# Optimization experiments

Hardware: AMD Instinct MI355X
Metric: run time of the kernel (lower is better)

Reference implementation:

```python
import jax, jax.numpy as jnp
import numpy as np


def setup_inputs() -> dict:
    key = jax.random.key(0)
    B, N, D = 8, 2048, 512
    put = jax.random.normal(key, (B, N, D), dtype=jnp.float32)
    return {"put": put, "k": 16}


def reference(put, k):
    # put: [B, N, D]; k: python int
    B, N, _ = put.shape
    # squared-norm expansion of pairwise Euclidean distance
    xx = jnp.sum(put * put, axis=2, keepdims=True)            # [B, N, 1]
    gram = jnp.einsum('bnd,bmd->bnm', put, put)               # [B, N, N]
    dist2 = xx + jnp.swapaxes(xx, 1, 2) - 2.0 * gram          # [B, N, N]
    dist = jnp.sqrt(jnp.clip(dist2, 0.0))                     # clamp(min=0).sqrt()

    # k nearest (smallest distance): top_k of negated distances
    _, inc = jax.lax.top_k(-dist, k)                          # [B, N, k] int32

    # binary adjacency: out[b, j, inc[b, j, :]] = 1 (vectorized scatter)
    b_idx = jnp.arange(B)[:, None, None]                      # [B,1,1]
    r_idx = jnp.arange(N)[None, :, None]                      # [1,N,1]
    out = jnp.zeros_like(dist).at[b_idx, r_idx, inc].set(1.0)
    return out
```

## Files before the change

kernel.cpp:

```cpp
#include <hip/hip_runtime.h>
#include <cstdint>

#define NN 2048
#define DD 512
#define NB 8
#define NCAND 24

using ull = unsigned long long;
typedef __attribute__((ext_vector_type(8))) short bf16x8;
typedef __attribute__((ext_vector_type(4))) float f32x4;

#define GLOAD_LDS16(g, l)                                                      \
  __builtin_amdgcn_global_load_lds(                                            \
      (const __attribute__((address_space(1))) unsigned int*)(g),              \
      (__attribute__((address_space(3))) unsigned int*)(l), 16, 0, 0)

__device__ inline unsigned short f2bf(float f) {
  unsigned u = __float_as_uint(f);
  unsigned r = u + 0x7FFFu + ((u >> 16) & 1u);
  return (unsigned short)(r >> 16);
}

#define CEX(a, i, j)                                                           \
  {                                                                            \
    unsigned lo_ = min(a[i], a[j]), hi_ = max(a[i], a[j]);                     \
    a[i] = lo_;                                                                \
    a[j] = hi_;                                                                \
  }

__device__ __forceinline__ void sort8(unsigned (&a)[8]) {
  CEX(a, 0, 1) CEX(a, 2, 3) CEX(a, 4, 5) CEX(a, 6, 7)
  CEX(a, 0, 2) CEX(a, 1, 3) CEX(a, 4, 6) CEX(a, 5, 7)
  CEX(a, 1, 2) CEX(a, 5, 6)
  CEX(a, 0, 4) CEX(a, 1, 5) CEX(a, 2, 6) CEX(a, 3, 7)
  CEX(a, 2, 4) CEX(a, 3, 5)
  CEX(a, 1, 2) CEX(a, 3, 4) CEX(a, 5, 6)
}

__device__ __forceinline__ void clean16(unsigned (&r)[16]) {
#pragma unroll
  for (int d = 8; d >= 1; d >>= 1) {
#pragma unroll
    for (int i = 0; i < 16; ++i)
      if ((i & d) == 0) CEX(r, i, i + d)
  }
}

__device__ __forceinline__ void merge16_full(const unsigned (&a)[8],
                                             const unsigned (&b)[8],
                                             unsigned (&r)[16]) {
#pragma unroll
  for (int i = 0; i < 8; ++i) { r[i] = a[i]; r[15 - i] = b[i]; }
  clean16(r);
}

__device__ __forceinline__ void top16(unsigned (&a)[16], const unsigned (&b)[16]) {
  unsigned t[16];
#pragma unroll
  for (int i = 0; i < 16; ++i) t[i] = min(a[i], b[15 - i]);
  clean16(t);
#pragma unroll
  for (int i = 0; i < 16; ++i) a[i] = t[i];
}

__device__ __forceinline__ void load8(unsigned (&a)[8], const unsigned short* p,
                                      unsigned c0) {
  uint4 u = *(const uint4*)p;
  a[0] = (u.x << 16) | c0;
  a[1] = (u.x & 0xFFFF0000u) | (c0 + 1);
  a[2] = (u.y << 16) | (c0 + 2);
  a[3] = (u.y & 0xFFFF0000u) | (c0 + 3);
  a[4] = (u.z << 16) | (c0 + 4);
  a[5] = (u.z & 0xFFFF0000u) | (c0 + 5);
  a[6] = (u.w << 16) | (c0 + 6);
  a[7] = (u.w & 0xFFFF0000u) | (c0 + 7);
}

__device__ __forceinline__ void sel_write(const unsigned short* S,
                                          unsigned* __restrict__ Kws, int b,
                                          int rowbase, int tile, int colbase,
                                          int t) {
  const int row = t >> 1, half = t & 1;
  const unsigned short* Sr = S + row * 136 + half * 64;
  const unsigned cb = (unsigned)(colbase + half * 64);
  unsigned m[16], s0[8], s1[8], n16[16];
  load8(s0, Sr + 0, cb + 0);
  load8(s1, Sr + 8, cb + 8);
  sort8(s0); sort8(s1);
  merge16_full(s0, s1, m);
#pragma unroll
  for (int c = 16; c < 64; c += 16) {
    load8(s0, Sr + c, cb + c);
    load8(s1, Sr + c + 8, cb + c + 8);
    sort8(s0); sort8(s1);
    merge16_full(s0, s1, n16);
    top16(m, n16);
  }
  unsigned o[16];
#pragma unroll
  for (int i = 0; i < 16; ++i) o[i] = (unsigned)__shfl_xor((int)m[i], 1, 64);
  top16(m, o);
  if (half == 0) {
    unsigned* dst = Kws + ((size_t)(b * NN + rowbase + row) * 16 + tile) * 12;
#pragma unroll
    for (int i = 0; i < 12; ++i) dst[i] = m[i];
  }
}

__global__ __launch_bounds__(256) void knn_prep(const float* __restrict__ put,
                                                float* __restrict__ norms32,
                                                unsigned short* __restrict__ bhalf) {
  const int row  = blockIdx.x * 4 + (threadIdx.x >> 6);
  const int lane = threadIdx.x & 63;
  const float* p = put + (size_t)row * DD + lane * 8;
  float4 x0 = ((const float4*)p)[0];
  float4 x1 = ((const float4*)p)[1];
  double s = (double)x0.x * (double)x0.x + (double)x0.y * (double)x0.y +
             (double)x0.z * (double)x0.z + (double)x0.w * (double)x0.w +
             (double)x1.x * (double)x1.x + (double)x1.y * (double)x1.y +
             (double)x1.z * (double)x1.z + (double)x1.w * (double)x1.w;
  uint4 v;
  v.x = (unsigned)f2bf(x0.x) | ((unsigned)f2bf(x0.y) << 16);
  v.y = (unsigned)f2bf(x0.z) | ((unsigned)f2bf(x0.w) << 16);
  v.z = (unsigned)f2bf(x1.x) | ((unsigned)f2bf(x1.y) << 16);
  v.w = (unsigned)f2bf(x1.z) | ((unsigned)f2bf(x1.w) << 16);
  *((uint4*)(bhalf + (size_t)row * DD) + lane) = v;
#pragma unroll
  for (int m = 1; m < 64; m <<= 1) s += __shfl_xor(s, m, 64);
  if (lane == 0) norms32[row] = (float)s;
}

__global__ __launch_bounds__(256, 3) void knn_gemm(
    const unsigned short* __restrict__ bhalf,
    const float* __restrict__ norms32,
    unsigned* __restrict__ Kws) {
  __shared__ unsigned short smem[17408];
  unsigned short* As = smem;
  unsigned short* Bs = smem + 4096;

  int idx = blockIdx.x;
  int jt = 0;
  while (idx >= 16 - jt) { idx -= 16 - jt; ++jt; }
  const int mt = jt + idx;

  const int t    = threadIdx.x;
  const int lane = t & 63;
  const int wv   = t >> 6;
  const int q    = lane >> 4;
  const int l15  = lane & 15;
  const int wrow = wv >> 1, wcol = wv & 1;
  const int m0 = mt * 128;
  const int j0 = jt * 128;
  const int b  = blockIdx.y;

  const unsigned short* pb = bhalf + (size_t)b * NN * DD;

  const int rloc = lane >> 2;
  const int kcg  = (lane & 3) ^ ((lane >> 3) & 3);
  const int i0 = 2 * wv, i1 = 2 * wv + 1;
  const unsigned short* gA0 = pb + (size_t)(j0 + 16 * i0 + rloc) * DD + kcg * 8;
  const unsigned short* gA1 = pb + (size_t)(j0 + 16 * i1 + rloc) * DD + kcg * 8;
  const unsigned short* gB0 = pb + (size_t)(m0 + 16 * i0 + rloc) * DD + kcg * 8;
  const unsigned short* gB1 = pb + (size_t)(m0 + 16 * i1 + rloc) * DD + kcg * 8;
  unsigned short* lA0 = As + i0 * 512;
  unsigned short* lA1 = As + i1 * 512;
  unsigned short* lB0 = Bs + i0 * 512;
  unsigned short* lB1 = Bs + i1 * 512;

  const int xsw = (q ^ ((l15 >> 1) & 3)) * 8;

  f32x4 acc[4][4];
  const f32x4 zz = {0.f, 0.f, 0.f, 0.f};
#pragma unroll
  for (int i = 0; i < 4; ++i)
#pragma unroll
    for (int j = 0; j < 4; ++j) acc[i][j] = zz;

  for (int kt = 0; kt < DD; kt += 32) {
    __syncthreads();
    GLOAD_LDS16(gA0, lA0);
    GLOAD_LDS16(gA1, lA1);
    GLOAD_LDS16(gB0, lB0);
    GLOAD_LDS16(gB1, lB1);
    gA0 += 32; gA1 += 32; gB0 += 32; gB1 += 32;
    __syncthreads();

    bf16x8 af[4], bg[4];
#pragma unroll
    for (int f = 0; f < 4; ++f) {
      af[f] = *(const bf16x8*)(As + (wrow * 64 + f * 16 + l15) * 32 + xsw);
      bg[f] = *(const bf16x8*)(Bs + (wcol * 64 + f * 16 + l15) * 32 + xsw);
    }
#pragma unroll
    for (int fi = 0; fi < 4; ++fi)
#pragma unroll
      for (int fj = 0; fj < 4; ++fj)
        acc[fi][fj] = __builtin_amdgcn_mfma_f32_16x16x32_bf16(
            af[fi], bg[fj], acc[fi][fj], 0, 0, 0);
  }

  float xn[4];
#pragma unroll
  for (int fj = 0; fj < 4; ++fj)
    xn[fj] = norms32[(size_t)b * NN + m0 + wcol * 64 + fj * 16 + l15];

  __syncthreads();
#pragma unroll
  for (int fi = 0; fi < 4; ++fi)
#pragma unroll
    for (int fj = 0; fj < 4; ++fj)
#pragma unroll
      for (int r = 0; r < 4; ++r) {
        float sv = xn[fj] - 2.0f * acc[fi][fj][r] + 2048.0f;
        smem[(wrow * 64 + fi * 16 + q * 4 + r) * 136 + wcol * 64 + fj * 16 + l15] =
            __builtin_bit_cast(unsigned short, (_Float16)sv);
      }
  __syncthreads();
  sel_write(smem, Kws, b, j0, mt, m0, t);

  if (jt != mt) {
    float xr[16];
#pragma unroll
    for (int fi = 0; fi < 4; ++fi)
#pragma unroll
      for (int r = 0; r < 4; ++r)
        xr[fi * 4 + r] =
            norms32[(size_t)b * NN + j0 + wrow * 64 + fi * 16 + q * 4 + r];

    __syncthreads();
#pragma unroll
    for (int fi = 0; fi < 4; ++fi)
#pragma unroll
      for (int fj = 0; fj < 4; ++fj)
#pragma unroll
        for (int r = 0; r < 4; ++r) {
          float sv = xr[fi * 4 + r] - 2.0f * acc[fi][fj][r] + 2048.0f;
          smem[(wcol * 64 + fj * 16 + l15) * 136 + wrow * 64 + fi * 16 + q * 4 + r] =
              __builtin_bit_cast(unsigned short, (_Float16)sv);
        }
    __syncthreads();
    sel_write(smem, Kws, b, m0, jt, j0, t);
  }
}

__global__ __launch_bounds__(256) void knn_select(
    const unsigned* __restrict__ Kws,
    const float* __restrict__ put,
    const float* __restrict__ norms32,
    float* __restrict__ out) {
  __shared__ unsigned candL[4][NCAND];
  __shared__ double part[4][NCAND][9];
  __shared__ ull keyL[4][NCAND];
  __shared__ unsigned winL[4][16];

  const int wv   = threadIdx.x >> 6;
  const int lane = threadIdx.x & 63;
  const int R = blockIdx.x * 4 + wv;
  const int b = R >> 11, j = R & (NN - 1);

  const unsigned* Krow = Kws + (size_t)R * 192 + lane * 3;
  unsigned h[3] = {Krow[0], Krow[1], Krow[2]};
  CEX(h, 0, 1) CEX(h, 1, 2) CEX(h, 0, 1)

#pragma unroll
  for (int pass = 0; pass < NCAND / 2; ++pass) {
    unsigned a1 = h[0], a2 = h[1];
#pragma unroll
    for (int m = 1; m < 64; m <<= 1) {
      unsigned b1 = (unsigned)__shfl_xor((int)a1, m, 64);
      unsigned b2 = (unsigned)__shfl_xor((int)a2, m, 64);
      unsigned lo  = min(a1, b1);
      unsigned mid = max(a1, b1);
      unsigned hi  = min(a2, b2);
      a1 = lo;
      a2 = min(mid, hi);
    }
    if ((h[0] == a1) | (h[0] == a2)) { h[0] = h[1]; h[1] = h[2]; h[2] = 0xFFFFFFFFu; }
    if (h[0] == a2)                  { h[0] = h[1]; h[1] = h[2]; h[2] = 0xFFFFFFFFu; }
    if (lane == 0) {
      candL[wv][2 * pass]     = a1 & 0xFFFFu;
      candL[wv][2 * pass + 1] = a2 & 0xFFFFu;
    }
  }

  const float* panel = put + (size_t)b * NN * DD;
  const float* xjp = panel + (size_t)j * DD + lane * 8;
  float4 xa = ((const float4*)xjp)[0];
  float4 xb = ((const float4*)xjp)[1];
  double x0 = xa.x, x1 = xa.y, x2 = xa.z, x3 = xa.w;
  double x4 = xb.x, x5 = xb.y, x6 = xb.z, x7 = xb.w;

  for (int c0 = 0; c0 < NCAND; c0 += 4) {
    double p[4];
#pragma unroll
    for (int uu = 0; uu < 4; ++uu) {
      int cand = __builtin_amdgcn_readfirstlane((int)candL[wv][c0 + uu]);
      const float4* cr = (const float4*)(panel + (size_t)cand * DD + lane * 8);
      float4 ya = cr[0];
      float4 yb = cr[1];
      p[uu] = x0 * (double)ya.x + x1 * (double)ya.y + x2 * (double)ya.z +
              x3 * (double)ya.w + x4 * (double)yb.x + x5 * (double)yb.y +
              x6 * (double)yb.z + x7 * (double)yb.w;
    }
#pragma unroll
    for (int uu = 0; uu < 4; ++uu) {
      p[uu] += __shfl_xor(p[uu], 1, 64);
      p[uu] += __shfl_xor(p[uu], 2, 64);
      p[uu] += __shfl_xor(p[uu], 4, 64);
      if ((lane & 7) == 0) part[wv][c0 + uu][lane >> 3] = p[uu];
    }
  }

  if (lane < NCAND) {
    double dot = part[wv][lane][0] + part[wv][lane][1] + part[wv][lane][2] +
                 part[wv][lane][3] + part[wv][lane][4] + part[wv][lane][5] +
                 part[wv][lane][6] + part[wv][lane][7];
    int cand = (int)candL[wv][lane];
    float g32 = (float)dot;
    float xxm = norms32[(size_t)b * NN + cand];
    float xxj = norms32[(size_t)b * NN + j];
    float s   = __fadd_rn(xxj, xxm);
    float d2  = __fsub_rn(s, __fmul_rn(2.0f, g32));
    d2 = fmaxf(d2, 0.0f);
    float dist = __fsqrt_rn(d2);
    keyL[wv][lane] = ((ull)__float_as_uint(dist) << 32) | (unsigned)cand;
  }
  if (lane < NCAND) {
    ull mine = keyL[wv][lane];
    int rank = 0;
#pragma unroll
    for (int i = 0; i < NCAND; ++i) rank += (keyL[wv][i] < mine) ? 1 : 0;
    if (rank < 16) winL[wv][rank] = (unsigned)(keyL[wv][lane] & 0xFFFFULL);
  }

  unsigned mask = 0;
#pragma unroll
  for (int i = 0; i < 16; ++i) {
    unsigned c = winL[wv][i];
    unsigned own = (((c >> 2) & 63u) == (unsigned)lane) ? 1u : 0u;
    unsigned bit = (((c >> 8) & 7u) << 2) | (c & 3u);
    mask |= own << bit;
  }
  float* orow = out + (size_t)R * NN;
#pragma unroll
  for (int it = 0; it < 8; ++it) {
    float4 v;
    v.x = (float)((mask >> (it * 4 + 0)) & 1u);
    v.y = (float)((mask >> (it * 4 + 1)) & 1u);
    v.z = (float)((mask >> (it * 4 + 2)) & 1u);
    v.w = (float)((mask >> (it * 4 + 3)) & 1u);
    ((float4*)(orow + it * 256))[lane] = v;
  }
}

extern "C" void kernel_launch(void* const* d_in, const int* in_sizes, int n_in,
                              void* d_out, int out_size, void* d_ws, size_t ws_size,
                              hipStream_t stream) {
  const float* put = (const float*)d_in[0];
  float* out = (float*)d_out;

  float* norms32 = (float*)d_ws;
  unsigned short* bhalf = (unsigned short*)((char*)d_ws + 65536);
  unsigned* Kws =
      (unsigned*)((char*)d_ws + 65536 + (size_t)NB * NN * DD * 2);

  knn_prep<<<dim3(NB * NN / 4), 256, 0, stream>>>(put, norms32, bhalf);
  knn_gemm<<<dim3(136, NB), 256, 0, stream>>>(bhalf, norms32, Kws);
  knn_select<<<dim3(NB * NN / 4), 256, 0, stream>>>(Kws, put, norms32, out);
}
```

Baseline: 249.4 us.

## Keep per-half top-8 candidates instead of merged top-12 per tile row

The per-tile selection now has each thread keep only the top 8 of its 64 columns using a cheaper 8-wide bitonic merge. It drops the 16-wide merges and the cross-lane shuffle that combined the two halves. Both halves write 8 keys each with vector stores, so the workspace grows to 256 keys per row and the final select loads 4 keys per lane. The LDS row stride goes from 136 to 138, presumably to change bank mapping, and the occupancy hint on the GEMM kernel is removed. The risk is that keeping 8 per half-tile instead of 12 per tile could miss true neighbours when they cluster within one 64-column half, and the workspace traffic is larger.

```diff
diff --git a/kernel.cpp b/kernel.cpp
--- a/kernel.cpp
+++ b/kernel.cpp
@@ -5,6 +5,7 @@
 #define DD 512
 #define NB 8
 #define NCAND 24
+#define SSTR 138
 
 using ull = unsigned long long;
 typedef __attribute__((ext_vector_type(8))) short bf16x8;
@@ -37,30 +38,15 @@
   CEX(a, 1, 2) CEX(a, 3, 4) CEX(a, 5, 6)
 }
 
-__device__ __forceinline__ void clean16(unsigned (&r)[16]) {
-#pragma unroll
-  for (int d = 8; d >= 1; d >>= 1) {
-#pragma unroll
-    for (int i = 0; i < 16; ++i)
-      if ((i & d) == 0) CEX(r, i, i + d)
-  }
-}
-
-__device__ __forceinline__ void merge16_full(const unsigned (&a)[8],
-                                             const unsigned (&b)[8],
-                                             unsigned (&r)[16]) {
-#pragma unroll
-  for (int i = 0; i < 8; ++i) { r[i] = a[i]; r[15 - i] = b[i]; }
-  clean16(r);
-}
-
-__device__ __forceinline__ void top16(unsigned (&a)[16], const unsigned (&b)[16]) {
-  unsigned t[16];
-#pragma unroll
-  for (int i = 0; i < 16; ++i) t[i] = min(a[i], b[15 - i]);
-  clean16(t);
-#pragma unroll
-  for (int i = 0; i < 16; ++i) a[i] = t[i];
+__device__ __forceinline__ void merge8(unsigned (&a)[8], const unsigned (&b)[8]) {
+  unsigned t[8];
+#pragma unroll
+  for (int i = 0; i < 8; ++i) t[i] = min(a[i], b[7 - i]);
+  CEX(t, 0, 4) CEX(t, 1, 5) CEX(t, 2, 6) CEX(t, 3, 7)
+  CEX(t, 0, 2) CEX(t, 1, 3) CEX(t, 4, 6) CEX(t, 5, 7)
+  CEX(t, 0, 1) CEX(t, 2, 3) CEX(t, 4, 5) CEX(t, 6, 7)
+#pragma unroll
+  for (int i = 0; i < 8; ++i) a[i] = t[i];
 }
 
 __device__ __forceinline__ void load8(unsigned (&a)[8], const unsigned short* p,
@@ -81,30 +67,24 @@
                                           int rowbase, int tile, int colbase,
                                           int t) {
   const int row = t >> 1, half = t & 1;
-  const unsigned short* Sr = S + row * 136 + half * 64;
+  const unsigned short* Sr = S + row * SSTR + half * 64;
   const unsigned cb = (unsigned)(colbase + half * 64);
-  unsigned m[16], s0[8], s1[8], n16[16];
-  load8(s0, Sr + 0, cb + 0);
-  load8(s1, Sr + 8, cb + 8);
-  sort8(s0); sort8(s1);
-  merge16_full(s0, s1, m);
-#pragma unroll
-  for (int c = 16; c < 64; c += 16) {
-    load8(s0, Sr + c, cb + c);
-    load8(s1, Sr + c + 8, cb + c + 8);
-    sort8(s0); sort8(s1);
-    merge16_full(s0, s1, n16);
-    top16(m, n16);
-  }
-  unsigned o[16];
-#pragma unroll
-  for (int i = 0; i < 16; ++i) o[i] = (unsigned)__shfl_xor((int)m[i], 1, 64);
-  top16(m, o);
-  if (half == 0) {
-    unsigned* dst = Kws + ((size_t)(b * NN + rowbase + row) * 16 + tile) * 12;
-#pragma unroll
-    for (int i = 0; i < 12; ++i) dst[i] = m[i];
-  }
+  unsigned m[8], s1[8];
+  load8(m, Sr, cb);
+  sort8(m);
+#pragma unroll
+  for (int c = 8; c < 64; c += 8) {
+    load8(s1, Sr + c, cb + c);
+    sort8(s1);
+    merge8(m, s1);
+  }
+  unsigned* dst =
+      Kws + (((size_t)(b * NN + rowbase + row) * 16 + tile) << 4) + half * 8;
+  uint4 v0, v1;
+  v0.x = m[0]; v0.y = m[1]; v0.z = m[2]; v0.w = m[3];
+  v1.x = m[4]; v1.y = m[5]; v1.z = m[6]; v1.w = m[7];
+  ((uint4*)dst)[0] = v0;
+  ((uint4*)dst)[1] = v1;
 }
 
 __global__ __launch_bounds__(256) void knn_prep(const float* __restrict__ put,
@@ -130,11 +110,11 @@
   if (lane == 0) norms32[row] = (float)s;
 }
 
-__global__ __launch_bounds__(256, 3) void knn_gemm(
+__global__ __launch_bounds__(256) void knn_gemm(
     const unsigned short* __restrict__ bhalf,
     const float* __restrict__ norms32,
     unsigned* __restrict__ Kws) {
-  __shared__ unsigned short smem[17408];
+  __shared__ unsigned short smem[17664];
   unsigned short* As = smem;
   unsigned short* Bs = smem + 4096;
 
@@ -212,7 +192,7 @@
 #pragma unroll
       for (int r = 0; r < 4; ++r) {
         float sv = xn[fj] - 2.0f * acc[fi][fj][r] + 2048.0f;
-        smem[(wrow * 64 + fi * 16 + q * 4 + r) * 136 + wcol * 64 + fj * 16 + l15] =
+        smem[(wrow * 64 + fi * 16 + q * 4 + r) * SSTR + wcol * 64 + fj * 16 + l15] =
             __builtin_bit_cast(unsigned short, (_Float16)sv);
       }
   __syncthreads();
@@ -235,7 +215,7 @@
 #pragma unroll
         for (int r = 0; r < 4; ++r) {
           float sv = xr[fi * 4 + r] - 2.0f * acc[fi][fj][r] + 2048.0f;
-          smem[(wcol * 64 + fj * 16 + l15) * 136 + wrow * 64 + fi * 16 + q * 4 + r] =
+          smem[(wcol * 64 + fj * 16 + l15) * SSTR + wrow * 64 + fi * 16 + q * 4 + r] =
               __builtin_bit_cast(unsigned short, (_Float16)sv);
         }
     __syncthreads();
@@ -258,9 +238,9 @@
   const int R = blockIdx.x * 4 + wv;
   const int b = R >> 11, j = R & (NN - 1);
 
-  const unsigned* Krow = Kws + (size_t)R * 192 + lane * 3;
-  unsigned h[3] = {Krow[0], Krow[1], Krow[2]};
-  CEX(h, 0, 1) CEX(h, 1, 2) CEX(h, 0, 1)
+  uint4 kv = *(const uint4*)(Kws + ((size_t)R << 8) + lane * 4);
+  unsigned h[4] = {kv.x, kv.y, kv.z, kv.w};
+  CEX(h, 0, 1) CEX(h, 2, 3) CEX(h, 0, 2) CEX(h, 1, 3) CEX(h, 1, 2)
 
 #pragma unroll
   for (int pass = 0; pass < NCAND / 2; ++pass) {
@@ -275,8 +255,12 @@
       a1 = lo;
       a2 = min(mid, hi);
     }
-    if ((h[0] == a1) | (h[0] == a2)) { h[0] = h[1]; h[1] = h[2]; h[2] = 0xFFFFFFFFu; }
-    if (h[0] == a2)                  { h[0] = h[1]; h[1] = h[2]; h[2] = 0xFFFFFFFFu; }
+    if ((h[0] == a1) | (h[0] == a2)) {
+      h[0] = h[1]; h[1] = h[2]; h[2] = h[3]; h[3] = 0xFFFFFFFFu;
+    }
+    if (h[0] == a2) {
+      h[0] = h[1]; h[1] = h[2]; h[2] = h[3]; h[3] = 0xFFFFFFFFu;
+    }
     if (lane == 0) {
       candL[wv][2 * pass]     = a1 & 0xFFFFu;
       candL[wv][2 * pass + 1] = a2 & 0xFFFFu;
```

After: 252.3 us. About the same (+1.1%).
